# Kernel optimization log

Hardware: AMD Instinct MI355X
Metric: run time of the kernel (lower is better)

## Reference

```python
import jax, jax.numpy as jnp
import numpy as np
import math

# config constants (match init_kwargs)
N_HEAD = 16
KNN_NUM = 4
MEM_FRAC = 4.0
BOOKKEEPING_FRAC = 0.0
RESID_ONLY = False
RESID_FOUND = 0.5   # set_resid_frac(resid_frac): found/current mix
RESID_CURR = 0.5
KNN_INFLUENCE = 1.0
NEG_INF = jnp.finfo(jnp.float32).min


def setup_inputs() -> dict:
    key = jax.random.key(0)
    k1, k2, k3, k4, k5 = jax.random.split(key, 5)
    B, T, C = 1, 2048, 1024
    H, d = N_HEAD, C // N_HEAD
    M = 8192  # per-head memory-store entries
    return {
        "x": jax.random.normal(k1, (B, T, C), jnp.float32),
        "c_attn_w": jax.random.normal(k2, (3 * C, C), jnp.float32) * 0.02,
        "c_proj_w": jax.random.normal(k3, (C, C), jnp.float32) * 0.02,
        "key_store": jax.random.normal(k4, (H, M, d), jnp.float32),
        "value_store": jax.random.normal(k5, (H, M, d), jnp.float32),
    }


def _knn_get(att, k, q, v, key_store, value_store):
    # att: (B,H,T,T), k/q/v: (B,H,T,d), stores: (H,M,d). B must be 1 (original
    # scatter offset i*t is only consistent for b==1).
    B, H, T, d = k.shape
    scale = 1.0 / math.sqrt(d)
    att_last = att[:, :, -1, :]                     # (B,H,T) last-query column
    # bookkeeping_frac == 0.0 -> skipped; mem_frac truthy -> threshold filter
    mask = att_last >= (1.0 / (MEM_FRAC * T))       # nonzero after zeroing

    # per-head flattened token lists, shape (H, N=B*T, d)
    kh = jnp.swapaxes(k, 0, 1).reshape(H, B * T, d)
    qh = jnp.swapaxes(q, 0, 1).reshape(H, B * T, d)
    vh = jnp.swapaxes(v, 0, 1).reshape(H, B * T, d)
    mask_h = jnp.swapaxes(mask, 0, 1).reshape(H, B * T)

    # exact L2 kNN (FAISS IndexFlatL2 equivalent): d2[h,n,m] = ||kh - ks||^2
    d2 = (jnp.sum(kh * kh, -1)[:, :, None]
          - 2.0 * jnp.einsum('hnd,hmd->hnm', kh, key_store)
          + jnp.sum(key_store * key_store, -1)[:, None, :])
    _, idx = jax.lax.top_k(-d2, KNN_NUM)            # (H,N,K) nearest indices

    h_ix = jnp.arange(H)[:, None, None]
    keys_found = key_store[h_ix, idx]               # (H,N,K,d)
    vals_found = value_store[h_ix, idx]
    keys_found = jnp.moveaxis(keys_found, 2, 0)     # (K,H,N,d)
    vals_found = jnp.moveaxis(vals_found, 2, 0)
    if not RESID_ONLY:
        keys_found = jnp.concatenate([kh[None], keys_found], axis=0)  # (K+1,H,N,d)
        vals_found = jnp.concatenate([vh[None], vals_found], axis=0)

    attf = jnp.einsum('khnd,hnd->khn', keys_found, qh) * scale
    attf = jnp.where(jnp.isnan(attf), NEG_INF, attf)
    attf = jax.nn.softmax(attf * KNN_INFLUENCE, axis=0)
    vals_new = jnp.einsum('khn,khnd->hnd', attf, vals_found)
    if RESID_FOUND > 0 or RESID_CURR > 0:
        vals_new = vals_new * RESID_FOUND + vh * RESID_CURR

    v_out = jnp.where(mask_h[..., None], vals_new, vh)   # scatter-equivalent
    return jnp.swapaxes(v_out.reshape(H, B, T, d), 0, 1)  # (B,H,T,d)


def reference(x, c_attn_w, c_proj_w, key_store, value_store):
    B, T, C = x.shape
    H, d = N_HEAD, C // N_HEAD
    qkv = x @ c_attn_w.T                             # (B,T,3C)
    q, k, v = jnp.split(qkv, 3, axis=2)
    q = jnp.swapaxes(q.reshape(B, T, H, d), 1, 2)    # (B,H,T,d)
    k = jnp.swapaxes(k.reshape(B, T, H, d), 1, 2)
    v = jnp.swapaxes(v.reshape(B, T, H, d), 1, 2)

    att = jnp.einsum('bhqd,bhkd->bhqk', q, k) * (1.0 / math.sqrt(d))
    causal = jnp.tril(jnp.ones((T, T), bool))
    att = jnp.where(causal, att, NEG_INF)
    att = jax.nn.softmax(att, axis=-1)

    # knn_get is @torch.no_grad() in the original -> stop_gradient
    v_new = jax.lax.stop_gradient(
        _knn_get(att, k, q, v, key_store, value_store))

    y = jnp.einsum('bhqk,bhkd->bhqd', att, v_new)
    y = jnp.swapaxes(y, 1, 2).reshape(B, T, C)
    return y @ c_proj_w.T
```

## Files before the change

kernel.cpp:

```cpp
#include <hip/hip_runtime.h>
#include <hip/hip_bf16.h>
#include <math.h>

#define TT 2048
#define CC 1024
#define HH 16
#define DDIM 64
#define MM 8192
#define C3 3072
#define SBIAS 256.0f

typedef __bf16 bf16x8 __attribute__((ext_vector_type(8)));
typedef float f32x4 __attribute__((ext_vector_type(4)));

__device__ __forceinline__ float waveReduceSum(float v) {
#pragma unroll
  for (int off = 32; off > 0; off >>= 1) v += __shfl_xor(v, off, 64);
  return v;
}
__device__ __forceinline__ unsigned umn(unsigned a, unsigned b){ return a<b?a:b; }
__device__ __forceinline__ unsigned umed3(unsigned a, unsigned b, unsigned c){
  unsigned d;
  asm("v_med3_u32 %0, %1, %2, %3" : "=v"(d) : "v"(a), "v"(b), "v"(c));
  return d;
}

__device__ __forceinline__ void gload16(const void* g, void* l) {
  __builtin_amdgcn_global_load_lds(
      (const __attribute__((address_space(1))) unsigned int*)g,
      (__attribute__((address_space(3))) unsigned int*)l, 16, 0, 0);
}

__global__ __launch_bounds__(256) void conv_split_k(const float* __restrict__ src,
    __hip_bfloat16* __restrict__ hi, __hip_bfloat16* __restrict__ lo)
{
  size_t i = (size_t)blockIdx.x*256 + threadIdx.x;
  const float4* p = (const float4*)(src + i*8);
  float4 a = p[0], b = p[1];
  float v[8] = {a.x,a.y,a.z,a.w,b.x,b.y,b.z,b.w};
  bf16x8 H, L;
#pragma unroll
  for (int e = 0; e < 8; ++e) {
    __bf16 hb = (__bf16)v[e];
    H[e] = hb;
    L[e] = (__bf16)(v[e] - (float)hb);
  }
  *reinterpret_cast<bf16x8*>(hi + i*8) = H;
  *reinterpret_cast<bf16x8*>(lo + i*8) = L;
}

__global__ __launch_bounds__(256) void conv_bf16_k(const float* __restrict__ src,
    __hip_bfloat16* __restrict__ dst)
{
  size_t i = (size_t)blockIdx.x*256 + threadIdx.x;
  const float4* p = (const float4*)(src + i*8);
  float4 a = p[0], b = p[1];
  float v[8] = {a.x,a.y,a.z,a.w,b.x,b.y,b.z,b.w};
  bf16x8 H;
#pragma unroll
  for (int e = 0; e < 8; ++e) H[e] = (__bf16)v[e];
  *reinterpret_cast<bf16x8*>(dst + i*8) = H;
}

__global__ __launch_bounds__(256) void conv_ks_k(const float* __restrict__ ks,
    __hip_bfloat16* __restrict__ ksb, float* __restrict__ ksn, float* __restrict__ ksnb)
{
  int row = blockIdx.x*4 + (threadIdx.x>>6);
  int lane = threadIdx.x & 63;
  float v = ks[(size_t)row*64 + lane];
  float sq = waveReduceSum(v*v);
  ksb[(size_t)row*64 + lane] = __float2bfloat16(v);
  if (lane == 0) { ksn[row] = sq; ksnb[row] = sq + SBIAS; }
}

__global__ __launch_bounds__(256) void conv_kb_k(const float* __restrict__ qkv,
    __hip_bfloat16* __restrict__ kb)
{
  int e = blockIdx.x*256 + threadIdx.x;
  int dg = e & 7; int t = (e>>3) & (TT-1); int h = e >> 14;
  const float* src = qkv + (size_t)t*C3 + CC + h*64 + dg*8;
  __hip_bfloat16* dst = kb + ((size_t)(h*TT + t)*64 + dg*8);
#pragma unroll
  for (int i = 0; i < 8; ++i) dst[i] = __float2bfloat16(src[i]);
}

__global__ __launch_bounds__(256) void vtrans_k(const float* __restrict__ vnew,
    __hip_bfloat16* __restrict__ vbT)
{
  __shared__ float tbuf[64][65];
  const int h = blockIdx.y, t0 = blockIdx.x*64, tid = threadIdx.x;
#pragma unroll
  for (int r = 0; r < 16; ++r) {
    int e = r*256 + tid; int row = e>>6, dv = e&63;
    tbuf[row][dv] = vnew[((size_t)h*TT + t0 + row)*64 + dv];
  }
  __syncthreads();
#pragma unroll
  for (int r = 0; r < 16; ++r) {
    int e = r*256 + tid; int dv = e>>6, tt = e&63;
    vbT[((size_t)h*64 + dv)*TT + t0 + tt] = __float2bfloat16(tbuf[tt][dv]);
  }
}

template<bool SPLIT>
__global__ __launch_bounds__(256) void gemm_mfma_k(
    const __hip_bfloat16* __restrict__ Ah, const __hip_bfloat16* __restrict__ Al,
    const __hip_bfloat16* __restrict__ Bh, const __hip_bfloat16* __restrict__ Bl,
    float* __restrict__ Cc, int M, int N, int K)
{
  __shared__ __align__(16) char lds[2][32768];
  const int tid = threadIdx.x;
  const int nbx = N >> 7;
  const int by = blockIdx.x / nbx, bx = blockIdx.x - by*nbx;
  const int m0 = by << 7, n0 = bx << 7;
  const int w = tid >> 6;
  const int l = tid & 63;
  const int wslot = w << 6;
  const int wi = w >> 1, wj = w & 1;
  const int fr = l & 15, fo = l >> 4;
  const int kw = SPLIT ? 32 : 64;
  const int nsteps = K / kw;

  f32x4 acc[4][4];
#pragma unroll
  for (int i = 0; i < 4; ++i)
#pragma unroll
    for (int j = 0; j < 4; ++j) acc[i][j] = f32x4{0.f,0.f,0.f,0.f};

  int srow[4], schg[4];
#pragma unroll
  for (int r = 0; r < 4; ++r) {
    int s = r*256 + tid;
    srow[r] = s >> 3;
    schg[r] = (s & 7) ^ (srow[r] & 7);
  }

  auto stageAB = [&](int buf, int st) {
    const int k0 = st * kw;
#pragma unroll
    for (int r = 0; r < 4; ++r) {
      const __hip_bfloat16 *pa, *pb;
      if (SPLIT) {
        pa = (schg[r] < 4 ? Ah : Al) + (size_t)(m0+srow[r])*K + k0 + (schg[r]&3)*8;
        pb = (schg[r] < 4 ? Bh : Bl) + (size_t)(n0+srow[r])*K + k0 + (schg[r]&3)*8;
      } else {
        pa = Ah + (size_t)(m0+srow[r])*K + k0 + schg[r]*8;
        pb = Bh + (size_t)(n0+srow[r])*K + k0 + schg[r]*8;
      }
      gload16(pa, lds[buf] + (r*256 + wslot)*16);
      gload16(pb, lds[buf] + 16384 + (r*256 + wslot)*16);
    }
  };

  stageAB(0, 0);
  __syncthreads();

  for (int st = 0; st < nsteps; ++st) {
    const int buf = st & 1;
    if (st + 1 < nsteps) stageAB(buf ^ 1, st + 1);
    char* ldsb = lds[buf];

    if (SPLIT) {
      bf16x8 bhf[4], blf[4];
#pragma unroll
      for (int j = 0; j < 4; ++j) {
        int row = wj*64 + j*16 + fr;
        bhf[j] = *(const bf16x8*)(ldsb + 16384 + row*128 + ((fo     ^ (row&7))*16));
        blf[j] = *(const bf16x8*)(ldsb + 16384 + row*128 + (((4+fo) ^ (row&7))*16));
      }
#pragma unroll
      for (int i = 0; i < 4; ++i) {
        int row = wi*64 + i*16 + fr;
        bf16x8 ah = *(const bf16x8*)(ldsb + row*128 + ((fo     ^ (row&7))*16));
        bf16x8 al = *(const bf16x8*)(ldsb + row*128 + (((4+fo) ^ (row&7))*16));
#pragma unroll
        for (int j = 0; j < 4; ++j) {
          acc[i][j] = __builtin_amdgcn_mfma_f32_16x16x32_bf16(al, bhf[j], acc[i][j], 0,0,0);
          acc[i][j] = __builtin_amdgcn_mfma_f32_16x16x32_bf16(ah, blf[j], acc[i][j], 0,0,0);
          acc[i][j] = __builtin_amdgcn_mfma_f32_16x16x32_bf16(ah, bhf[j], acc[i][j], 0,0,0);
        }
      }
    } else {
#pragma unroll
      for (int kk = 0; kk < 2; ++kk) {
        bf16x8 bf[4];
#pragma unroll
        for (int j = 0; j < 4; ++j) {
          int row = wj*64 + j*16 + fr;
          bf[j] = *(const bf16x8*)(ldsb + 16384 + row*128 + (((kk*4+fo) ^ (row&7))*16));
        }
#pragma unroll
        for (int i = 0; i < 4; ++i) {
          int row = wi*64 + i*16 + fr;
          bf16x8 af = *(const bf16x8*)(ldsb + row*128 + (((kk*4+fo) ^ (row&7))*16));
#pragma unroll
          for (int j = 0; j < 4; ++j)
            acc[i][j] = __builtin_amdgcn_mfma_f32_16x16x32_bf16(af, bf[j], acc[i][j], 0,0,0);
        }
      }
    }
    __syncthreads();
  }

  float* ep = (float*)((char*)lds + (size_t)w*8704);
#pragma unroll
  for (int pass = 0; pass < 2; ++pass) {
#pragma unroll
    for (int ii = 0; ii < 2; ++ii) {
      int i = pass*2 + ii;
#pragma unroll
      for (int j = 0; j < 4; ++j)
#pragma unroll
        for (int e = 0; e < 4; ++e)
          ep[(ii*16 + fo*4 + e)*68 + j*16 + fr] = acc[i][j][e];
    }
#pragma unroll
    for (int eidx = 0; eidx < 8; ++eidx) {
      int fi = eidx*64 + l;
      int row = fi >> 4, c4 = fi & 15;
      float4 v4 = *(const float4*)(ep + row*68 + c4*4);
      *(float4*)(Cc + (size_t)(m0 + wi*64 + pass*32 + row)*N + n0 + wj*64 + c4*4) = v4;
    }
  }
}

__global__ __launch_bounds__(256) void attlast_mask_k(const float* __restrict__ qkv, int* __restrict__ mask)
{
  const int h = blockIdx.x;
  __shared__ float ql[64];
  __shared__ float lg[TT];
  __shared__ float red[256];
  const int tid = threadIdx.x;
  if (tid < 64) ql[tid] = qkv[(size_t)(TT-1)*C3 + h*DDIM + tid];
  __syncthreads();
  float lmax = -INFINITY;
  for (int t = tid; t < TT; t += 256) {
    const float* kr = qkv + (size_t)t*C3 + CC + h*DDIM;
    float s = 0.f;
#pragma unroll
    for (int d = 0; d < 64; ++d) s += ql[d] * kr[d];
    s *= 0.125f;
    lg[t] = s;
    lmax = fmaxf(lmax, s);
  }
  red[tid] = lmax; __syncthreads();
  for (int off = 128; off > 0; off >>= 1) { if (tid < off) red[tid] = fmaxf(red[tid], red[tid+off]); __syncthreads(); }
  float mx = red[0];
  __syncthreads();
  float ls = 0.f;
  for (int t = tid; t < TT; t += 256) { float e = expf(lg[t]-mx); lg[t] = e; ls += e; }
  red[tid] = ls; __syncthreads();
  for (int off = 128; off > 0; off >>= 1) { if (tid < off) red[tid] += red[tid+off]; __syncthreads(); }
  float Z = red[0];
  for (int t = tid; t < TT; t += 256) mask[h*TT + t] = (lg[t]/Z >= 1.220703125e-4f) ? 1 : 0;
}

__global__ __launch_bounds__(256) void knn_chunkmin_k(
    const __hip_bfloat16* __restrict__ kb, const __hip_bfloat16* __restrict__ ksb,
    const float* __restrict__ ksnb, unsigned int* __restrict__ cand)
{
  __shared__ __align__(16) char lds[32768];
  const int tid = threadIdx.x;
  const int bid = blockIdx.x;
  const int orig = (bid & 7)*128 + (bid >> 3);
  const int h  = orig >> 6;
  const int n0 = (orig & 63) * 32;
  const int w  = tid >> 6;
  const int wh = w >> 1;
  const int wr = w & 1;
  const int l  = tid & 63;
  const int cr = l & 15, hi = l >> 4;

  bf16x8 af0, af1;
  {
    const __hip_bfloat16* kbh = kb + (size_t)h*TT*64 + (size_t)(n0 + wr*16 + cr)*64;
    af0 = *reinterpret_cast<const bf16x8*>(kbh + hi*8);
    af1 = *reinterpret_cast<const bf16x8*>(kbh + 32 + hi*8);
  }
  const __hip_bfloat16* ksbh = ksb + (size_t)h*MM*64;
  const float* ksnh = ksnb + (size_t)h*MM;

  char* myhalf = lds + wh*16384;
  int gsrc[4];
#pragma unroll
  for (int r = 0; r < 4; ++r) {
    int s = r*128 + wr*64 + l;
    gsrc[r] = (s & ~7) | ((s & 7) ^ ((s >> 3) & 7));
  }
  const int rb0 = cr*128 + ((hi ^ (l&7))*16);
  const int rb1 = cr*128 + (((4+hi) ^ (l&7))*16);

  unsigned cnd[4][4];
#pragma unroll
  for (int i = 0; i < 4; ++i)
#pragma unroll
    for (int c = 0; c < 4; ++c) cnd[i][c] = 0xFFFFFFFFu;

  auto stage = [&](int buf, int tt) {
    const __hip_bfloat16* src = ksbh + ((size_t)(wh*64 + tt))*4096;
    char* dst = myhalf + buf*8192 + (wr << 10);
#pragma unroll
    for (int r = 0; r < 4; ++r)
      gload16(src + gsrc[r]*8, dst + (r << 11));
  };

  stage(0, 0);
  __syncthreads();

  for (int tt = 0; tt < 64; ++tt) {
    const int buf = tt & 1;
    if (tt + 1 < 64) stage(buf ^ 1, tt + 1);
    char* ldsb = myhalf + buf*8192;
    const int ttg = wh*64 + tt;
    const unsigned crtt = ((unsigned)cr << 7) | (unsigned)ttg;

    float kn0 = ksnh[ttg*64 +  0 + cr];
    float kn1 = ksnh[ttg*64 + 16 + cr];
    float kn2 = ksnh[ttg*64 + 32 + cr];
    float kn3 = ksnh[ttg*64 + 48 + cr];

    f32x4 acc[4];
#pragma unroll
    for (int b = 0; b < 4; ++b) {
      bf16x8 bf0 = *reinterpret_cast<const bf16x8*>(ldsb + b*2048 + rb0);
      bf16x8 bf1 = *reinterpret_cast<const bf16x8*>(ldsb + b*2048 + rb1);
      f32x4 z = {0.f, 0.f, 0.f, 0.f};
      z = __builtin_amdgcn_mfma_f32_16x16x32_bf16(af0, bf0, z, 0, 0, 0);
      z = __builtin_amdgcn_mfma_f32_16x16x32_bf16(af1, bf1, z, 0, 0, 0);
      acc[b] = z;
    }
#pragma unroll
    for (int i = 0; i < 4; ++i) {
      float s0 = fmaf(acc[0][i], -2.f, kn0);
      float s1 = fmaf(acc[1][i], -2.f, kn1);
      float s2 = fmaf(acc[2][i], -2.f, kn2);
      float s3 = fmaf(acc[3][i], -2.f, kn3);
      float m4 = fminf(fminf(s0, s1), fminf(s2, s3));
      unsigned x = (__float_as_uint(m4) & 0xFFFFF800u) | crtt;
      unsigned t0 = umn(cnd[i][0], x);
      unsigned t1 = umed3(x, cnd[i][0], cnd[i][1]);
      unsigned t2 = umed3(x, cnd[i][1], cnd[i][2]);
      unsigned t3 = umed3(x, cnd[i][2], cnd[i][3]);
      cnd[i][0] = t0; cnd[i][1] = t1; cnd[i][2] = t2; cnd[i][3] = t3;
    }
    __syncthreads();
  }

  uint4* sh = (uint4*)lds;
  if (wh == 1) {
#pragma unroll
    for (int i = 0; i < 4; ++i)
      sh[wr*256 + (hi*4+i)*16 + cr] = make_uint4(cnd[i][0], cnd[i][1], cnd[i][2], cnd[i][3]);
  }
  __syncthreads();
  if (wh == 0) {
#pragma unroll
    for (int i = 0; i < 4; ++i) {
      uint4 b = sh[wr*256 + (hi*4+i)*16 + cr];
      int n = n0 + wr*16 + hi*4 + i;
      reinterpret_cast<uint4*>(cand)[(size_t)(h*TT + n)*16 + cr] =
          make_uint4(umn(cnd[i][0], b.w), umn(cnd[i][1], b.z),
                     umn(cnd[i][2], b.y), umn(cnd[i][3], b.x));
    }
  }
}

__global__ __launch_bounds__(256) void knn_fused_k(
    const unsigned int* __restrict__ cand, const float* __restrict__ qkv,
    const float* __restrict__ kstore, const float* __restrict__ vstore,
    const float* __restrict__ ksn, const int* __restrict__ mask,
    float* __restrict__ vnew)
{
  const int row = blockIdx.x*4 + (threadIdx.x>>6);
  const int l = threadIdx.x & 63;
  const int ll = l & 31;
  const int h = row >> 11, t = row & (TT-1);
  const float* base = qkv + (size_t)t*C3 + h*64;
  float vh = base[2*CC + l];
  float* outp = vnew + (size_t)row*64;
  if (!mask[row]) { outp[l] = vh; return; }

  unsigned v = cand[(size_t)row*64 + l];
#pragma unroll
  for (int k = 2; k <= 64; k <<= 1)
#pragma unroll
    for (int j = k>>1; j > 0; j >>= 1) {
      unsigned o = __shfl_xor(v, j, 64);
      bool takeMin = ((l & j) == 0) == ((l & k) == 0);
      v = (takeMin == (o < v)) ? o : v;
    }

  const int c = l >> 1;
  const int b = c & 3;
  unsigned vc = __shfl(v, c >> 2, 64);
  const int m = ((int)(vc & 127u))*64 + b*16 + (int)((vc >> 7) & 15u);
  const int p = l & 1;
  unsigned kh, km;
  {
    const float* kq = base + CC + p*32;
    const float* ksr = kstore + ((size_t)h*MM + m)*64 + p*32;
    float dp = 0.f;
#pragma unroll
    for (int i = 0; i < 8; ++i) {
      float4 a = *(const float4*)(kq + i*4);
      float4 bb = *(const float4*)(ksr + i*4);
      dp = fmaf(a.x,bb.x, fmaf(a.y,bb.y, fmaf(a.z,bb.z, fmaf(a.w,bb.w, dp))));
    }
    dp += __shfl_xor(dp, 1, 64);
    float s = ksn[(size_t)h*MM + m] - 2.f*dp;
    unsigned u = __float_as_uint(s);
    unsigned skey = u ^ (unsigned)(((int)u >> 31) | 0x80000000);
    kh = __shfl(skey, 2*ll, 64);
    km = __shfl((unsigned)m, 2*ll, 64);
#pragma unroll
    for (int k = 2; k <= 32; k <<= 1)
#pragma unroll
      for (int j = k>>1; j > 0; j >>= 1) {
        unsigned oh = __shfl_xor(kh, j, 64);
        unsigned ol = __shfl_xor(km, j, 64);
        bool takeMin = ((ll & j) == 0) == ((ll & k) == 0);
        bool oLess = (oh < kh) || (oh == kh && ol < km);
        if (takeMin == oLess) { kh = oh; km = ol; }
      }
  }

  const int m0 = (int)__shfl(km, 0, 64);
  const int m1 = (int)__shfl(km, 1, 64);
  const int m2 = (int)__shfl(km, 2, 64);
  const int m3 = (int)__shfl(km, 3, 64);
  const int g = l >> 3, gl = l & 7;
  float dq = 0.f;
  if (g < 5) {
    int msel = (g == 0) ? m0 : (g == 1) ? m1 : (g == 2) ? m2 : m3;
    const float* qrow = base + gl*8;
    const float* kr = (g < 4) ? (kstore + ((size_t)h*MM + msel)*64 + gl*8)
                              : (base + CC + gl*8);
    float4 a0 = *(const float4*)(qrow);
    float4 a1 = *(const float4*)(qrow + 4);
    float4 b0 = *(const float4*)(kr);
    float4 b1 = *(const float4*)(kr + 4);
    dq = a0.x*b0.x + a0.y*b0.y + a0.z*b0.z + a0.w*b0.w
       + a1.x*b1.x + a1.y*b1.y + a1.z*b1.z + a1.w*b1.w;
  }
  dq += __shfl_xor(dq, 1, 64);
  dq += __shfl_xor(dq, 2, 64);
  dq += __shfl_xor(dq, 4, 64);
  float d0 = __shfl(dq,  0, 64)*0.125f;
  float d1 = __shfl(dq,  8, 64)*0.125f;
  float d2 = __shfl(dq, 16, 64)*0.125f;
  float d3 = __shfl(dq, 24, 64)*0.125f;
  float d4 = __shfl(dq, 32, 64)*0.125f;
  float mx = fmaxf(fmaxf(fmaxf(d0,d1),fmaxf(d2,d3)),d4);
  float w0 = __expf(d0-mx), w1 = __expf(d1-mx), w2 = __expf(d2-mx),
        w3 = __expf(d3-mx), w4 = __expf(d4-mx);
  float Z = w0+w1+w2+w3+w4;
  float vv = w4*vh
           + w0*vstore[((size_t)h*MM+m0)*64 + l]
           + w1*vstore[((size_t)h*MM+m1)*64 + l]
           + w2*vstore[((size_t)h*MM+m2)*64 + l]
           + w3*vstore[((size_t)h*MM+m3)*64 + l];
  outp[l] = 0.5f*(vv/Z) + 0.5f*vh;
}

__global__ __launch_bounds__(256) void attn_mfma_k(
    const float* __restrict__ qkv, const __hip_bfloat16* __restrict__ kb,
    const __hip_bfloat16* __restrict__ vbT, __hip_bfloat16* __restrict__ yb)
{
  __shared__ __align__(16) char lds[40960];
  const int h = blockIdx.y, bx = blockIdx.x, tid = threadIdx.x;
  const int w = tid>>6, l = tid&63, fr = l&15, fo = l>>4;
  const int wslot = w << 6;
  const __hip_bfloat16* kbh = kb + (size_t)h*TT*64;
  const __hip_bfloat16* vbh = vbT + (size_t)h*64*TT;
  char* Pt = lds + 32768 + w*2048;

  int srow[2], schg[2];
#pragma unroll
  for (int r = 0; r < 2; ++r) {
    int s = r*256 + tid;
    srow[r] = s >> 3;
    schg[r] = (s & 7) ^ (srow[r] & 7);
  }

  auto stageKV = [&](int buf, int kt) {
#pragma unroll
    for (int r = 0; r < 2; ++r) {
      gload16(kbh + (size_t)(kt*64 + srow[r])*64 + schg[r]*8,
              lds + buf*16384 + (r*256 + wslot)*16);
      gload16(vbh + (size_t)srow[r]*TT + kt*64 + schg[r]*8,
              lds + buf*16384 + 8192 + (r*256 + wslot)*16);
    }
  };

  const int qblk = 31 - bx;
  const int q0 = qblk * 64;
  bf16x8 qa[2];
  {
    const float* qrow = qkv + (size_t)(q0 + w*16 + fr)*C3 + h*64;
#pragma unroll
    for (int kk = 0; kk < 2; ++kk) {
      float4 u0 = *(const float4*)(qrow + kk*32 + fo*8);
      float4 u1 = *(const float4*)(qrow + kk*32 + fo*8 + 4);
      bf16x8 t;
      t[0]=(__bf16)u0.x; t[1]=(__bf16)u0.y; t[2]=(__bf16)u0.z; t[3]=(__bf16)u0.w;
      t[4]=(__bf16)u1.x; t[5]=(__bf16)u1.y; t[6]=(__bf16)u1.z; t[7]=(__bf16)u1.w;
      qa[kk] = t;
    }
  }
  float mrow[4], lsum[4];
  f32x4 oacc[4];
#pragma unroll
  for (int e = 0; e < 4; ++e) { mrow[e] = -INFINITY; lsum[e] = 0.f; }
#pragma unroll
  for (int jv = 0; jv < 4; ++jv) oacc[jv] = f32x4{0.f,0.f,0.f,0.f};

  const int ntiles = qblk + 1;
  stageKV(0, 0);
  __syncthreads();

  for (int kt = 0; kt < ntiles; ++kt) {
    const int buf = kt & 1;
    if (kt + 1 < ntiles) stageKV(buf ^ 1, kt + 1);
    char* Kt = lds + buf*16384;
    char* Vt = Kt + 8192;

    f32x4 sv[4];
#pragma unroll
    for (int j = 0; j < 4; ++j) {
      int row = j*16 + fr;
      bf16x8 k0f = *(const bf16x8*)(Kt + row*128 + ((fo     ^ (row&7))*16));
      bf16x8 k1f = *(const bf16x8*)(Kt + row*128 + (((4+fo) ^ (row&7))*16));
      f32x4 z = {0.f,0.f,0.f,0.f};
      z = __builtin_amdgcn_mfma_f32_16x16x32_bf16(qa[0], k0f, z, 0,0,0);
      z = __builtin_amdgcn_mfma_f32_16x16x32_bf16(qa[1], k1f, z, 0,0,0);
      sv[j] = z;
    }
    if (kt == qblk) {
#pragma unroll
      for (int j = 0; j < 4; ++j)
#pragma unroll
        for (int e = 0; e < 4; ++e)
          sv[j][e] = (j*16 + fr <= w*16 + fo*4 + e) ? sv[j][e]*0.125f : -INFINITY;
    } else {
#pragma unroll
      for (int j = 0; j < 4; ++j)
#pragma unroll
        for (int e = 0; e < 4; ++e) sv[j][e] *= 0.125f;
    }
    float rmax[4];
#pragma unroll
    for (int e = 0; e < 4; ++e)
      rmax[e] = fmaxf(fmaxf(sv[0][e], sv[1][e]), fmaxf(sv[2][e], sv[3][e]));
#pragma unroll
    for (int off = 1; off < 16; off <<= 1)
#pragma unroll
      for (int e = 0; e < 4; ++e) rmax[e] = fmaxf(rmax[e], __shfl_xor(rmax[e], off, 64));
    float scl[4];
#pragma unroll
    for (int e = 0; e < 4; ++e) {
      float mn = fmaxf(mrow[e], rmax[e]);
      scl[e] = __expf(mrow[e] - mn);
      mrow[e] = mn;
    }
    float rsum[4] = {0.f,0.f,0.f,0.f};
#pragma unroll
    for (int j = 0; j < 4; ++j) {
      int chunkbase = j*2 + (fr>>3);
      int kvoff = (fr&7)*2;
#pragma unroll
      for (int e = 0; e < 4; ++e) {
        float p = __expf(sv[j][e] - mrow[e]);
        rsum[e] += p;
        int qloc = fo*4 + e;
        *(__bf16*)(Pt + qloc*128 + ((chunkbase ^ (qloc&7))*16) + kvoff) = (__bf16)p;
      }
    }
#pragma unroll
    for (int off = 1; off < 16; off <<= 1)
#pragma unroll
      for (int e = 0; e < 4; ++e) rsum[e] += __shfl_xor(rsum[e], off, 64);
#pragma unroll
    for (int e = 0; e < 4; ++e) lsum[e] = lsum[e]*scl[e] + rsum[e];
#pragma unroll
    for (int jv = 0; jv < 4; ++jv)
#pragma unroll
      for (int e = 0; e < 4; ++e) oacc[jv][e] *= scl[e];

    bf16x8 pa0 = *(const bf16x8*)(Pt + fr*128 + ((fo     ^ (fr&7))*16));
    bf16x8 pa1 = *(const bf16x8*)(Pt + fr*128 + (((4+fo) ^ (fr&7))*16));
#pragma unroll
    for (int jv = 0; jv < 4; ++jv) {
      int row = jv*16 + fr;
      bf16x8 v0f = *(const bf16x8*)(Vt + row*128 + ((fo     ^ (row&7))*16));
      bf16x8 v1f = *(const bf16x8*)(Vt + row*128 + (((4+fo) ^ (row&7))*16));
      oacc[jv] = __builtin_amdgcn_mfma_f32_16x16x32_bf16(pa0, v0f, oacc[jv], 0,0,0);
      oacc[jv] = __builtin_amdgcn_mfma_f32_16x16x32_bf16(pa1, v1f, oacc[jv], 0,0,0);
    }
    __syncthreads();
  }
#pragma unroll
  for (int jv = 0; jv < 4; ++jv)
#pragma unroll
    for (int e = 0; e < 4; ++e) {
      int t = q0 + w*16 + fo*4 + e;
      yb[(size_t)t*CC + h*64 + jv*16 + fr] = __float2bfloat16(oacc[jv][e] / lsum[e]);
    }
}

extern "C" void kernel_launch(void* const* d_in, const int* in_sizes, int n_in,
                              void* d_out, int out_size, void* d_ws, size_t ws_size,
                              hipStream_t stream) {
  const float* x   = (const float*)d_in[0];
  const float* wat = (const float*)d_in[1];
  const float* wpr = (const float*)d_in[2];
  const float* kst = (const float*)d_in[3];
  const float* vst = (const float*)d_in[4];
  float* out = (float*)d_out;

  float* ws    = (float*)d_ws;
  float* qkv   = ws;
  float* ksn   = qkv + (size_t)6291456;
  float* ksnb  = ksn + 131072;
  int*   idxb  = (int*)(ksnb + 131072);
  int*   maskb = idxb + 131072;
  __hip_bfloat16* kb = (__hip_bfloat16*)(maskb + 32768);
  float* candRegion = (float*)kb + 1048576;
  unsigned int* candb = (unsigned int*)candRegion;
  float* vnew = candRegion;
  __hip_bfloat16* vbT = (__hip_bfloat16*)(candRegion + 2097152);
  float* split = candRegion + 2097152 + 1048576;
  __hip_bfloat16* xhi = (__hip_bfloat16*)split;
  __hip_bfloat16* xlo = xhi + 2097152;
  __hip_bfloat16* whi = xlo + 2097152;
  __hip_bfloat16* wlo = whi + 3145728;
  __hip_bfloat16* ksb  = (__hip_bfloat16*)split;
  __hip_bfloat16* wprb = ksb + 8388608;
  __hip_bfloat16* yb   = (__hip_bfloat16*)split;

  conv_split_k<<<dim3(1024), 256, 0, stream>>>(x, xhi, xlo);
  conv_split_k<<<dim3(1536), 256, 0, stream>>>(wat, whi, wlo);
  gemm_mfma_k<true><<<dim3(16*24), 256, 0, stream>>>(xhi, xlo, whi, wlo, qkv, TT, C3, CC);
  conv_kb_k<<<dim3(1024), 256, 0, stream>>>(qkv, kb);
  conv_ks_k<<<dim3(HH*MM/4), 256, 0, stream>>>(kst, ksb, ksn, ksnb);
  conv_bf16_k<<<dim3(512), 256, 0, stream>>>(wpr, wprb);
  attlast_mask_k<<<dim3(HH), 256, 0, stream>>>(qkv, maskb);
  knn_chunkmin_k<<<dim3(1024), 256, 0, stream>>>(kb, ksb, ksnb, candb);
  knn_fused_k<<<dim3(HH*TT/4), 256, 0, stream>>>(candb, qkv, kst, vst, ksn, maskb, vnew);
  vtrans_k<<<dim3(32, HH), 256, 0, stream>>>(vnew, vbT);
  attn_mfma_k<<<dim3(32, HH), 256, 0, stream>>>(qkv, kb, vbT, yb);
  gemm_mfma_k<false><<<dim3(16*8), 256, 0, stream>>>(yb, nullptr, wprb, nullptr, out, TT, CC, CC);
}
```

Baseline: 314.3 us.

## Use split-bf16 precision only for K projection, plain bf16 for Q and V

```diff
diff --git a/kernel.cpp b/kernel.cpp
--- a/kernel.cpp
+++ b/kernel.cpp
@@ -19,11 +19,7 @@
   return v;
 }
 __device__ __forceinline__ unsigned umn(unsigned a, unsigned b){ return a<b?a:b; }
-__device__ __forceinline__ unsigned umed3(unsigned a, unsigned b, unsigned c){
-  unsigned d;
-  asm("v_med3_u32 %0, %1, %2, %3" : "=v"(d) : "v"(a), "v"(b), "v"(c));
-  return d;
-}
+__device__ __forceinline__ unsigned umx(unsigned a, unsigned b){ return a>b?a:b; }
 
 __device__ __forceinline__ void gload16(const void* g, void* l) {
   __builtin_amdgcn_global_load_lds(
@@ -84,21 +80,21 @@
   for (int i = 0; i < 8; ++i) dst[i] = __float2bfloat16(src[i]);
 }
 
-__global__ __launch_bounds__(256) void vtrans_k(const float* __restrict__ vnew,
+__global__ __launch_bounds__(256) void vtrans_k(const __hip_bfloat16* __restrict__ vnewb,
     __hip_bfloat16* __restrict__ vbT)
 {
-  __shared__ float tbuf[64][65];
+  __shared__ __hip_bfloat16 tbuf[64][65];
   const int h = blockIdx.y, t0 = blockIdx.x*64, tid = threadIdx.x;
 #pragma unroll
   for (int r = 0; r < 16; ++r) {
     int e = r*256 + tid; int row = e>>6, dv = e&63;
-    tbuf[row][dv] = vnew[((size_t)h*TT + t0 + row)*64 + dv];
+    tbuf[row][dv] = vnewb[((size_t)h*TT + t0 + row)*64 + dv];
   }
   __syncthreads();
 #pragma unroll
   for (int r = 0; r < 16; ++r) {
     int e = r*256 + tid; int dv = e>>6, tt = e&63;
-    vbT[((size_t)h*64 + dv)*TT + t0 + tt] = __float2bfloat16(tbuf[tt][dv]);
+    vbT[((size_t)h*64 + dv)*TT + t0 + tt] = tbuf[tt][dv];
   }
 }
 
@@ -106,7 +102,7 @@
 __global__ __launch_bounds__(256) void gemm_mfma_k(
     const __hip_bfloat16* __restrict__ Ah, const __hip_bfloat16* __restrict__ Al,
     const __hip_bfloat16* __restrict__ Bh, const __hip_bfloat16* __restrict__ Bl,
-    float* __restrict__ Cc, int M, int N, int K)
+    float* __restrict__ Cc, int M, int N, int K, int ldc)
 {
   __shared__ __align__(16) char lds[2][32768];
   const int tid = threadIdx.x;
@@ -132,7 +128,7 @@
   for (int r = 0; r < 4; ++r) {
     int s = r*256 + tid;
     srow[r] = s >> 3;
-    schg[r] = (s & 7) ^ (srow[r] & 7);
+    schg[r] = (s & 7) ^ ((s >> 3) & 7);
   }
 
   auto stageAB = [&](int buf, int st) {
@@ -219,19 +215,35 @@
       int fi = eidx*64 + l;
       int row = fi >> 4, c4 = fi & 15;
       float4 v4 = *(const float4*)(ep + row*68 + c4*4);
-      *(float4*)(Cc + (size_t)(m0 + wi*64 + pass*32 + row)*N + n0 + wj*64 + c4*4) = v4;
-    }
-  }
-}
-
-__global__ __launch_bounds__(256) void attlast_mask_k(const float* __restrict__ qkv, int* __restrict__ mask)
+      *(float4*)(Cc + (size_t)(m0 + wi*64 + pass*32 + row)*ldc + n0 + wj*64 + c4*4) = v4;
+    }
+  }
+}
+
+__global__ __launch_bounds__(256) void attlast_mask_k(
+    const float* __restrict__ x, const float* __restrict__ wat,
+    const float* __restrict__ qkv, int* __restrict__ mask)
 {
   const int h = blockIdx.x;
   __shared__ float ql[64];
   __shared__ float lg[TT];
   __shared__ float red[256];
   const int tid = threadIdx.x;
-  if (tid < 64) ql[tid] = qkv[(size_t)(TT-1)*C3 + h*DDIM + tid];
+  {
+    const int dd = tid >> 2, qd = tid & 3;
+    const float* xr = x + (size_t)(TT-1)*CC + qd*256;
+    const float* wr = wat + (size_t)(h*64 + dd)*CC + qd*256;
+    float s = 0.f;
+#pragma unroll 16
+    for (int i = 0; i < 64; ++i) {
+      float4 a = *(const float4*)(xr + i*4);
+      float4 b = *(const float4*)(wr + i*4);
+      s = fmaf(a.x,b.x, fmaf(a.y,b.y, fmaf(a.z,b.z, fmaf(a.w,b.w, s))));
+    }
+    s += __shfl_xor(s, 1, 64);
+    s += __shfl_xor(s, 2, 64);
+    if (qd == 0) ql[dd] = s;
+  }
   __syncthreads();
   float lmax = -INFINITY;
   for (int t = tid; t < TT; t += 256) {
@@ -335,13 +347,13 @@
       float s1 = fmaf(acc[1][i], -2.f, kn1);
       float s2 = fmaf(acc[2][i], -2.f, kn2);
       float s3 = fmaf(acc[3][i], -2.f, kn3);
-      float m4 = fminf(fminf(s0, s1), fminf(s2, s3));
+      float m4 = fminf(fminf(fminf(s0, s1), s2), s3);
       unsigned x = (__float_as_uint(m4) & 0xFFFFF800u) | crtt;
-      unsigned t0 = umn(cnd[i][0], x);
-      unsigned t1 = umed3(x, cnd[i][0], cnd[i][1]);
-      unsigned t2 = umed3(x, cnd[i][1], cnd[i][2]);
-      unsigned t3 = umed3(x, cnd[i][2], cnd[i][3]);
-      cnd[i][0] = t0; cnd[i][1] = t1; cnd[i][2] = t2; cnd[i][3] = t3;
+      unsigned c0 = cnd[i][0], c1 = cnd[i][1], c2 = cnd[i][2], c3 = cnd[i][3];
+      cnd[i][0] = umn(c0, x);
+      cnd[i][1] = umn(umx(x, c0), c1);
+      cnd[i][2] = umn(umx(x, c1), c2);
+      cnd[i][3] = umn(umx(x, c2), c3);
     }
     __syncthreads();
   }
@@ -369,7 +381,7 @@
     const unsigned int* __restrict__ cand, const float* __restrict__ qkv,
     const float* __restrict__ kstore, const float* __restrict__ vstore,
     const float* __restrict__ ksn, const int* __restrict__ mask,
-    float* __restrict__ vnew)
+    __hip_bfloat16* __restrict__ vnewb)
 {
   const int row = blockIdx.x*4 + (threadIdx.x>>6);
   const int l = threadIdx.x & 63;
@@ -377,8 +389,8 @@
   const int h = row >> 11, t = row & (TT-1);
   const float* base = qkv + (size_t)t*C3 + h*64;
   float vh = base[2*CC + l];
-  float* outp = vnew + (size_t)row*64;
-  if (!mask[row]) { outp[l] = vh; return; }
+  __hip_bfloat16* outp = vnewb + (size_t)row*64;
+  if (!mask[row]) { outp[l] = __float2bfloat16(vh); return; }
 
   unsigned v = cand[(size_t)row*64 + l];
 #pragma unroll
@@ -459,7 +471,7 @@
            + w1*vstore[((size_t)h*MM+m1)*64 + l]
            + w2*vstore[((size_t)h*MM+m2)*64 + l]
            + w3*vstore[((size_t)h*MM+m3)*64 + l];
-  outp[l] = 0.5f*(vv/Z) + 0.5f*vh;
+  outp[l] = __float2bfloat16(0.5f*(vv/Z) + 0.5f*vh);
 }
 
 __global__ __launch_bounds__(256) void attn_mfma_k(
@@ -479,7 +491,7 @@
   for (int r = 0; r < 2; ++r) {
     int s = r*256 + tid;
     srow[r] = s >> 3;
-    schg[r] = (s & 7) ^ (srow[r] & 7);
+    schg[r] = (s & 7) ^ ((s >> 3) & 7);
   }
 
   auto stageKV = [&](int buf, int kt) {
@@ -621,32 +633,37 @@
   float* qkv   = ws;
   float* ksn   = qkv + (size_t)6291456;
   float* ksnb  = ksn + 131072;
-  int*   idxb  = (int*)(ksnb + 131072);
-  int*   maskb = idxb + 131072;
+  int*   maskb = (int*)(ksnb + 131072);
   __hip_bfloat16* kb = (__hip_bfloat16*)(maskb + 32768);
   float* candRegion = (float*)kb + 1048576;
   unsigned int* candb = (unsigned int*)candRegion;
-  float* vnew = candRegion;
   __hip_bfloat16* vbT = (__hip_bfloat16*)(candRegion + 2097152);
   float* split = candRegion + 2097152 + 1048576;
-  __hip_bfloat16* xhi = (__hip_bfloat16*)split;
-  __hip_bfloat16* xlo = xhi + 2097152;
-  __hip_bfloat16* whi = xlo + 2097152;
-  __hip_bfloat16* wlo = whi + 3145728;
-  __hip_bfloat16* ksb  = (__hip_bfloat16*)split;
-  __hip_bfloat16* wprb = ksb + 8388608;
-  __hip_bfloat16* yb   = (__hip_bfloat16*)split;
+  __hip_bfloat16* xhi  = (__hip_bfloat16*)split;
+  __hip_bfloat16* xlo  = xhi + 2097152;
+  __hip_bfloat16* whiK = xlo + 2097152;
+  __hip_bfloat16* wloK = whiK + 1048576;
+  __hip_bfloat16* wqb  = wloK + 1048576;
+  __hip_bfloat16* wvb  = wqb + 1048576;
+  __hip_bfloat16* ksb   = (__hip_bfloat16*)split;
+  __hip_bfloat16* wprb  = ksb + 8388608;
+  __hip_bfloat16* vnewb = (__hip_bfloat16*)split;
+  __hip_bfloat16* yb    = (__hip_bfloat16*)split;
 
   conv_split_k<<<dim3(1024), 256, 0, stream>>>(x, xhi, xlo);
-  conv_split_k<<<dim3(1536), 256, 0, stream>>>(wat, whi, wlo);
-  gemm_mfma_k<true><<<dim3(16*24), 256, 0, stream>>>(xhi, xlo, whi, wlo, qkv, TT, C3, CC);
+  conv_split_k<<<dim3(512), 256, 0, stream>>>(wat + (size_t)CC*CC, whiK, wloK);
+  conv_bf16_k<<<dim3(512), 256, 0, stream>>>(wat, wqb);
+  conv_bf16_k<<<dim3(512), 256, 0, stream>>>(wat + (size_t)2*CC*CC, wvb);
+  gemm_mfma_k<false><<<dim3(128), 256, 0, stream>>>(xhi, nullptr, wqb, nullptr, qkv,        TT, CC, CC, C3);
+  gemm_mfma_k<true ><<<dim3(128), 256, 0, stream>>>(xhi, xlo, whiK, wloK,      qkv + CC,   TT, CC, CC, C3);
+  gemm_mfma_k<false><<<dim3(128), 256, 0, stream>>>(xhi, nullptr, wvb, nullptr, qkv + 2*CC, TT, CC, CC, C3);
   conv_kb_k<<<dim3(1024), 256, 0, stream>>>(qkv, kb);
   conv_ks_k<<<dim3(HH*MM/4), 256, 0, stream>>>(kst, ksb, ksn, ksnb);
   conv_bf16_k<<<dim3(512), 256, 0, stream>>>(wpr, wprb);
-  attlast_mask_k<<<dim3(HH), 256, 0, stream>>>(qkv, maskb);
+  attlast_mask_k<<<dim3(HH), 256, 0, stream>>>(x, wat, qkv, maskb);
   knn_chunkmin_k<<<dim3(1024), 256, 0, stream>>>(kb, ksb, ksnb, candb);
-  knn_fused_k<<<dim3(HH*TT/4), 256, 0, stream>>>(candb, qkv, kst, vst, ksn, maskb, vnew);
-  vtrans_k<<<dim3(32, HH), 256, 0, stream>>>(vnew, vbT);
+  knn_fused_k<<<dim3(HH*TT/4), 256, 0, stream>>>(candb, qkv, kst, vst, ksn, maskb, vnewb);
+  vtrans_k<<<dim3(32, HH), 256, 0, stream>>>(vnewb, vbT);
   attn_mfma_k<<<dim3(32, HH), 256, 0, stream>>>(qkv, kb, vbT, yb);
-  gemm_mfma_k<false><<<dim3(16*8), 256, 0, stream>>>(yb, nullptr, wprb, nullptr, out, TT, CC, CC);
-}
+  gemm_mfma_k<false><<<dim3(128), 256, 0, stream>>>(yb, nullptr, wprb, nullptr, out, TT, CC, CC, CC);
+}
```

After: 350.7 us. 1.12x slower.
